# Optimization experiments

Measured on AMD Instinct MI355X. Metric: run time of the kernel, lower is better.

## Reference

```python
import jax, jax.numpy as jnp
import numpy as np

B, N, C, H = 4, 1024, 768, 12
D = C // H
SCALE = D ** -0.5


def setup_inputs() -> dict:
    key = jax.random.key(0)
    k1, k2, k3, k4 = jax.random.split(key, 4)
    x1 = jax.random.normal(k1, (B, N, C), dtype=jnp.float32)
    x2 = jax.random.normal(k2, (B, N, C), dtype=jnp.float32)
    # shared (dual-stream) Linear2 weights, torch nn.Linear layout: [out, in]
    W_qkv = jax.random.normal(k3, (3 * C, C), dtype=jnp.float32) * (C ** -0.5)
    b_qkv = jnp.zeros((3 * C,), dtype=jnp.float32)
    W_proj = jax.random.normal(k4, (C, C), dtype=jnp.float32) * (C ** -0.5)
    b_proj = jnp.zeros((C,), dtype=jnp.float32)
    return {"x1": x1, "x2": x2, "W_qkv": W_qkv, "b_qkv": b_qkv,
            "W_proj": W_proj, "b_proj": b_proj}


def _split_qkv(x, W_qkv, b_qkv):
    qkv = (x @ W_qkv.T + b_qkv).reshape(B, N, 3, H, D)
    qkv = jnp.transpose(qkv, (2, 0, 3, 1, 4))  # [3,B,H,N,D]
    return qkv[0], qkv[1], qkv[2]


def reference(x1, x2, W_qkv, b_qkv, W_proj, b_proj):
    q1, k1, v1 = _split_qkv(x1, W_qkv, b_qkv)
    q2, k2, v2 = _split_qkv(x2, W_qkv, b_qkv)
    # two score maps, combined before a single shared softmax
    s1 = jnp.einsum("bhqd,bhkd->bhqk", q1 * SCALE, k1)
    s2 = jnp.einsum("bhqd,bhkd->bhqk", q2 * SCALE, k2)
    attn = jax.nn.softmax(s1 + s2, axis=-1)  # [B,H,N,N]
    # same attention matrix applied to both value streams
    o1 = jnp.einsum("bhqk,bhkd->bhqd", attn, v1)
    o2 = jnpum = jnp.einsum("bhqk,bhkd->bhqd", attn, v2) if False else jnp.einsum("bhqk,bhkd->bhqd", attn, v2)
    o1 = jnp.transpose(o1, (0, 2, 1, 3)).reshape(B, N, C)
    o2 = jnp.transpose(o2, (0, 2, 1, 3)).reshape(B, N, C)
    y1 = o1 @ W_proj.T + b_proj
    y2 = o2 @ W_proj.T + b_proj
    return y1, y2
```

## Files before the change

### kernel.cpp

```cpp
#include <hip/hip_runtime.h>
#include <hip/hip_bf16.h>


typedef __bf16 bf16x8 __attribute__((ext_vector_type(8)));
typedef float  f32x4  __attribute__((ext_vector_type(4)));

__device__ __forceinline__ bf16x8 cvt8(const float* p) {
    f32x4 f0 = *(const f32x4*)p;
    f32x4 f1 = *(const f32x4*)(p + 4);
    bf16x8 r;
    r[0] = (__bf16)f0[0]; r[1] = (__bf16)f0[1]; r[2] = (__bf16)f0[2]; r[3] = (__bf16)f0[3];
    r[4] = (__bf16)f1[0]; r[5] = (__bf16)f1[1]; r[6] = (__bf16)f1[2]; r[7] = (__bf16)f1[3];
    return r;
}

__device__ __forceinline__ void async16(const __bf16* g, __bf16* l) {
    __builtin_amdgcn_global_load_lds(
        (const __attribute__((address_space(1))) void*)g,
        (__attribute__((address_space(3))) void*)l, 16, 0, 0);
}

__global__ __launch_bounds__(256)
void cvt_k(const float* __restrict__ src, __bf16* __restrict__ dst, int n) {
    int i = (blockIdx.x * 256 + threadIdx.x) * 8;
    if (i < n) *(bf16x8*)(dst + i) = cvt8(src + i);
}

__global__ __launch_bounds__(256)
void gemm_qkv_s(const __bf16* __restrict__ A, const __bf16* __restrict__ Wq,
                const float* __restrict__ bias,
                __bf16* __restrict__ qo, __bf16* __restrict__ ko,
                __bf16* __restrict__ vo, int st)
{
    constexpr int K = 768;
    __shared__ __bf16 As[128 * 32];
    __shared__ __bf16 Bs[128 * 32];

    const int t = threadIdx.x, w = t >> 6, lane = t & 63;
    const int l15 = lane & 15, quad = lane >> 4;
    const int wm = w >> 1, wn = w & 1;
    const int gx = blockIdx.x, gy = blockIdx.y;
    const int lrow = lane >> 2, lcol = (lane & 3) * 8;

    const __bf16* Ab = A  + (size_t)(gy * 128) * K;
    const __bf16* Bb = Wq + (size_t)(gx * 128) * K;

    f32x4 acc[4][4];
#pragma unroll
    for (int mi = 0; mi < 4; mi++)
#pragma unroll
        for (int ni = 0; ni < 4; ni++) acc[mi][ni] = f32x4{0.f, 0.f, 0.f, 0.f};

    for (int k0 = 0; k0 < K; k0 += 32) {
#pragma unroll
        for (int i = 0; i < 2; i++) {
            int r = w * 32 + i * 16 + lrow;
            async16(Ab + (size_t)r * K + k0 + lcol, &As[r * 32 + lcol]);
            async16(Bb + (size_t)r * K + k0 + lcol, &Bs[r * 32 + lcol]);
        }
        __syncthreads();
        bf16x8 af[4], bfr[4];
#pragma unroll
        for (int mi = 0; mi < 4; mi++)
            af[mi] = *(const bf16x8*)&As[(wm * 64 + mi * 16 + l15) * 32 + quad * 8];
#pragma unroll
        for (int ni = 0; ni < 4; ni++)
            bfr[ni] = *(const bf16x8*)&Bs[(wn * 64 + ni * 16 + l15) * 32 + quad * 8];
#pragma unroll
        for (int mi = 0; mi < 4; mi++)
#pragma unroll
            for (int ni = 0; ni < 4; ni++)
                acc[mi][ni] = __builtin_amdgcn_mfma_f32_16x16x32_bf16(af[mi], bfr[ni], acc[mi][ni], 0, 0, 0);
        __syncthreads();
    }

#pragma unroll
    for (int ni = 0; ni < 4; ni++) {
        int j     = gx * 128 + wn * 64 + ni * 16 + l15;
        int which = j / 768;
        int c     = j - which * 768;
        int h = c >> 6, d = c & 63;
        float bj  = bias[j];
#pragma unroll
        for (int mi = 0; mi < 4; mi++) {
#pragma unroll
            for (int r = 0; r < 4; r++) {
                int row = gy * 128 + wm * 64 + mi * 16 + quad * 4 + r;
                int b = row >> 10, tok = row & 1023;
                float val = acc[mi][ni][r] + bj;
                if (which == 0)
                    qo[((size_t)((st * 4 + b) * 12 + h) * 1024 + tok) * 64 + d] = (__bf16)(val * 0.125f);
                else if (which == 1)
                    ko[((size_t)((st * 4 + b) * 12 + h) * 1024 + tok) * 64 + d] = (__bf16)val;
                else
                    vo[((size_t)((st * 4 + b) * 12 + h) * 64 + d) * 1024 + tok] = (__bf16)val;
            }
        }
    }
}

__global__ __launch_bounds__(256)
void gemm_proj(const __bf16* __restrict__ A, const __bf16* __restrict__ Wp,
               const float* __restrict__ bias, float* __restrict__ out)
{
    constexpr int K = 768;
    __shared__ __bf16 As[128 * 32];
    __shared__ __bf16 Bs[128 * 32];

    const int t = threadIdx.x, w = t >> 6, lane = t & 63;
    const int l15 = lane & 15, quad = lane >> 4;
    const int wm = w >> 1, wn = w & 1;
    const int gx = blockIdx.x, gy = blockIdx.y;
    const int lrow = lane >> 2, lcol = (lane & 3) * 8;

    const __bf16* Ab = A  + (size_t)(gy * 128) * K;
    const __bf16* Bb = Wp + (size_t)(gx * 128) * K;

    f32x4 acc[4][4];
#pragma unroll
    for (int mi = 0; mi < 4; mi++)
#pragma unroll
        for (int ni = 0; ni < 4; ni++) acc[mi][ni] = f32x4{0.f, 0.f, 0.f, 0.f};

    for (int k0 = 0; k0 < K; k0 += 32) {
#pragma unroll
        for (int i = 0; i < 2; i++) {
            int r = w * 32 + i * 16 + lrow;
            async16(Ab + (size_t)r * K + k0 + lcol, &As[r * 32 + lcol]);
            async16(Bb + (size_t)r * K + k0 + lcol, &Bs[r * 32 + lcol]);
        }
        __syncthreads();
        bf16x8 af[4], bfr[4];
#pragma unroll
        for (int mi = 0; mi < 4; mi++)
            af[mi] = *(const bf16x8*)&As[(wm * 64 + mi * 16 + l15) * 32 + quad * 8];
#pragma unroll
        for (int ni = 0; ni < 4; ni++)
            bfr[ni] = *(const bf16x8*)&Bs[(wn * 64 + ni * 16 + l15) * 32 + quad * 8];
#pragma unroll
        for (int mi = 0; mi < 4; mi++)
#pragma unroll
            for (int ni = 0; ni < 4; ni++)
                acc[mi][ni] = __builtin_amdgcn_mfma_f32_16x16x32_bf16(af[mi], bfr[ni], acc[mi][ni], 0, 0, 0);
        __syncthreads();
    }

#pragma unroll
    for (int ni = 0; ni < 4; ni++) {
        int col  = gx * 128 + wn * 64 + ni * 16 + l15;
        float bj = bias[col];
#pragma unroll
        for (int mi = 0; mi < 4; mi++)
#pragma unroll
            for (int r = 0; r < 4; r++) {
                int row = gy * 128 + wm * 64 + mi * 16 + quad * 4 + r;
                out[(size_t)row * 768 + col] = acc[mi][ni][r] + bj;
            }
    }
}

__global__ __launch_bounds__(256)
void attn_k(const __bf16* __restrict__ qws, const __bf16* __restrict__ kws,
            const __bf16* __restrict__ vws, __bf16* __restrict__ ows)
{
    __shared__ __bf16 KVf[2][2][2][4][512];
    __shared__ __bf16 Ps[4][16 * 72];

    const int g  = blockIdx.x;
    const int qt = g / 48;
    const int bh = g % 48;
    const int b = bh / 12, h = bh % 12;
    const int t = threadIdx.x, w = t >> 6, lane = t & 63;
    const int l15 = lane & 15, quad = lane >> 4;

    const size_t head_off = (size_t)bh * 65536;
    const size_t ss       = (size_t)48 * 65536;

    bf16x8 qf[2][2];
#pragma unroll
    for (int s = 0; s < 2; s++)
#pragma unroll
        for (int kk = 0; kk < 2; kk++)
            qf[s][kk] = *(const bf16x8*)(qws + s * ss + head_off
                          + (size_t)(qt * 64 + w * 16 + l15) * 64 + kk * 32 + quad * 8);

    float m_prev = -1e30f, l_run = 0.f;
    f32x4 accO[2][4];
#pragma unroll
    for (int s = 0; s < 2; s++)
#pragma unroll
        for (int ni = 0; ni < 4; ni++) accO[s][ni] = f32x4{0.f, 0.f, 0.f, 0.f};

    const __bf16* kbase = kws + head_off;
    const __bf16* vbase = vws + head_off;

    for (int kt = 0; kt < 16; kt++) {
        __syncthreads();
#pragma unroll
        for (int i = 0; i < 8; i++) {
            int f  = w * 8 + i;
            int kv = f >> 4, s = (f >> 3) & 1, kk = (f >> 2) & 1, mi = f & 3;
            const __bf16* gp;
            if (kv == 0)
                gp = kbase + s * ss + (size_t)(kt * 64 + mi * 16 + l15) * 64
                     + kk * 32 + quad * 8;
            else
                gp = vbase + s * ss + (size_t)(mi * 16 + l15) * 1024
                     + kt * 64 + kk * 32 + quad * 8;
            async16(gp, &KVf[kv][s][kk][mi][lane * 8]);
        }
        __syncthreads();

        f32x4 accS[4];
#pragma unroll
        for (int i = 0; i < 4; i++) accS[i] = f32x4{0.f, 0.f, 0.f, 0.f};
#pragma unroll
        for (int s = 0; s < 2; s++)
#pragma unroll
            for (int kk = 0; kk < 2; kk++) {
                bf16x8 kf[4];
#pragma unroll
                for (int mi = 0; mi < 4; mi++)
                    kf[mi] = *(const bf16x8*)&KVf[0][s][kk][mi][lane * 8];
#pragma unroll
                for (int mi = 0; mi < 4; mi++)
                    accS[mi] = __builtin_amdgcn_mfma_f32_16x16x32_bf16(kf[mi], qf[s][kk], accS[mi], 0, 0, 0);
            }

        float mx = accS[0][0];
#pragma unroll
        for (int mi = 0; mi < 4; mi++)
#pragma unroll
            for (int r = 0; r < 4; r++) mx = fmaxf(mx, accS[mi][r]);
        mx = fmaxf(mx, __shfl_xor(mx, 16));
        mx = fmaxf(mx, __shfl_xor(mx, 32));
        float mnew  = fmaxf(m_prev, mx);
        float alpha = __expf(m_prev - mnew);
        float p[4][4], rs = 0.f;
#pragma unroll
        for (int mi = 0; mi < 4; mi++)
#pragma unroll
            for (int r = 0; r < 4; r++) {
                float pv = __expf(accS[mi][r] - mnew);
                p[mi][r] = pv;
                rs += pv;
            }
        rs += __shfl_xor(rs, 16);
        rs += __shfl_xor(rs, 32);
        l_run  = l_run * alpha + rs;
        m_prev = mnew;

        float alr[4];
#pragma unroll
        for (int r = 0; r < 4; r++) alr[r] = __shfl(alpha, quad * 4 + r);
#pragma unroll
        for (int s = 0; s < 2; s++)
#pragma unroll
            for (int ni = 0; ni < 4; ni++)
#pragma unroll
                for (int r = 0; r < 4; r++) accO[s][ni][r] *= alr[r];

#pragma unroll
        for (int mi = 0; mi < 4; mi++)
#pragma unroll
            for (int r = 0; r < 4; r++)
                Ps[w][l15 * 72 + mi * 16 + quad * 4 + r] = (__bf16)p[mi][r];

#pragma unroll
        for (int kk = 0; kk < 2; kk++) {
            bf16x8 pa = *(const bf16x8*)&Ps[w][l15 * 72 + kk * 32 + quad * 8];
#pragma unroll
            for (int s = 0; s < 2; s++)
#pragma unroll
                for (int ni = 0; ni < 4; ni++) {
                    bf16x8 vf = *(const bf16x8*)&KVf[1][s][kk][ni][lane * 8];
                    accO[s][ni] = __builtin_amdgcn_mfma_f32_16x16x32_bf16(pa, vf, accO[s][ni], 0, 0, 0);
                }
        }
    }

    float il = 1.f / l_run;
    float ilr[4];
#pragma unroll
    for (int r = 0; r < 4; r++) ilr[r] = __shfl(il, quad * 4 + r);
#pragma unroll
    for (int r = 0; r < 4; r++) {
        int tok = qt * 64 + w * 16 + quad * 4 + r;
#pragma unroll
        for (int s = 0; s < 2; s++)
#pragma unroll
            for (int ni = 0; ni < 4; ni++) {
                size_t idx = ((size_t)((s * 4 + b) * 1024 + tok)) * 768 + h * 64 + ni * 16 + l15;
                ows[idx] = (__bf16)(accO[s][ni][r] * ilr[r]);
            }
    }
}

extern "C" void kernel_launch(void* const* d_in, const int* in_sizes, int n_in,
                              void* d_out, int out_size, void* d_ws, size_t ws_size,
                              hipStream_t stream)
{
    const float* x1    = (const float*)d_in[0];
    const float* x2    = (const float*)d_in[1];
    const float* Wqkv  = (const float*)d_in[2];
    const float* bqkv  = (const float*)d_in[3];
    const float* Wproj = (const float*)d_in[4];
    const float* bproj = (const float*)d_in[5];
    float* out = (float*)d_out;

    const size_t qkv_elems = (size_t)2 * 4 * 12 * 1024 * 64;
    __bf16* q_ws = (__bf16*)d_ws;
    __bf16* k_ws = q_ws + qkv_elems;
    __bf16* v_ws = k_ws + qkv_elems;
    __bf16* pool = v_ws + qkv_elems;
    __bf16* Xc  = pool;
    __bf16* Wqc = pool + 3145728;
    __bf16* o_ws = pool;
    __bf16* Wpc = q_ws;

    cvt_k<<<1536, 256, 0, stream>>>(x1, Xc, 3145728);
    cvt_k<<<864,  256, 0, stream>>>(Wqkv, Wqc, 1769472);
    gemm_qkv_s<<<dim3(18, 32), 256, 0, stream>>>(Xc, Wqc, bqkv, q_ws, k_ws, v_ws, 0);
    cvt_k<<<1536, 256, 0, stream>>>(x2, Xc, 3145728);
    gemm_qkv_s<<<dim3(18, 32), 256, 0, stream>>>(Xc, Wqc, bqkv, q_ws, k_ws, v_ws, 1);
    attn_k<<<768, 256, 0, stream>>>(q_ws, k_ws, v_ws, o_ws);
    cvt_k<<<288, 256, 0, stream>>>(Wproj, Wpc, 589824);
    gemm_proj<<<dim3(6, 64), 256, 0, stream>>>(o_ws, Wpc, bproj, out);
}
```

Measured before the change: 250.1 us.

## Deepen GEMM K-tile to 64 and load V directly to registers in attention

Both GEMM kernels now stage a 64-wide K slice per iteration instead of 32, halving the number of barrier pairs and loop iterations while doubling LDS use. In the attention kernel, each wave loads V fragments straight from global memory into registers instead of going through shared memory, so only K is staged in LDS. P is written to LDS as packed 4-element bf16 vectors. The V change raises register pressure, and each wave now reads the full V tile redundantly from global or cache.

```diff
diff --git a/kernel.cpp b/kernel.cpp
--- a/kernel.cpp
+++ b/kernel.cpp
@@ -3,6 +3,7 @@
 
 
 typedef __bf16 bf16x8 __attribute__((ext_vector_type(8)));
+typedef __bf16 bf16x4 __attribute__((ext_vector_type(4)));
 typedef float  f32x4  __attribute__((ext_vector_type(4)));
 
 __device__ __forceinline__ bf16x8 cvt8(const float* p) {
@@ -33,14 +34,15 @@
                 __bf16* __restrict__ vo, int st)
 {
     constexpr int K = 768;
-    __shared__ __bf16 As[128 * 32];
-    __shared__ __bf16 Bs[128 * 32];
+    __shared__ __bf16 As[128 * 64];
+    __shared__ __bf16 Bs[128 * 64];
 
     const int t = threadIdx.x, w = t >> 6, lane = t & 63;
     const int l15 = lane & 15, quad = lane >> 4;
     const int wm = w >> 1, wn = w & 1;
     const int gx = blockIdx.x, gy = blockIdx.y;
-    const int lrow = lane >> 2, lcol = (lane & 3) * 8;
+    const int srow = w * 32 + (lane >> 3);
+    const int scol = (lane & 7) * 8;
 
     const __bf16* Ab = A  + (size_t)(gy * 128) * K;
     const __bf16* Bb = Wq + (size_t)(gx * 128) * K;
@@ -51,26 +53,29 @@
 #pragma unroll
         for (int ni = 0; ni < 4; ni++) acc[mi][ni] = f32x4{0.f, 0.f, 0.f, 0.f};
 
-    for (int k0 = 0; k0 < K; k0 += 32) {
-#pragma unroll
-        for (int i = 0; i < 2; i++) {
-            int r = w * 32 + i * 16 + lrow;
-            async16(Ab + (size_t)r * K + k0 + lcol, &As[r * 32 + lcol]);
-            async16(Bb + (size_t)r * K + k0 + lcol, &Bs[r * 32 + lcol]);
-        }
-        __syncthreads();
-        bf16x8 af[4], bfr[4];
-#pragma unroll
-        for (int mi = 0; mi < 4; mi++)
-            af[mi] = *(const bf16x8*)&As[(wm * 64 + mi * 16 + l15) * 32 + quad * 8];
-#pragma unroll
-        for (int ni = 0; ni < 4; ni++)
-            bfr[ni] = *(const bf16x8*)&Bs[(wn * 64 + ni * 16 + l15) * 32 + quad * 8];
-#pragma unroll
-        for (int mi = 0; mi < 4; mi++)
+    for (int k0 = 0; k0 < K; k0 += 64) {
+#pragma unroll
+        for (int i = 0; i < 4; i++) {
+            int r = srow + i * 8;
+            async16(Ab + (size_t)r * K + k0 + scol, &As[r * 64 + scol]);
+            async16(Bb + (size_t)r * K + k0 + scol, &Bs[r * 64 + scol]);
+        }
+        __syncthreads();
+#pragma unroll
+        for (int kk = 0; kk < 2; kk++) {
+            bf16x8 af[4], bfr[4];
+#pragma unroll
+            for (int mi = 0; mi < 4; mi++)
+                af[mi] = *(const bf16x8*)&As[(wm * 64 + mi * 16 + l15) * 64 + kk * 32 + quad * 8];
 #pragma unroll
             for (int ni = 0; ni < 4; ni++)
-                acc[mi][ni] = __builtin_amdgcn_mfma_f32_16x16x32_bf16(af[mi], bfr[ni], acc[mi][ni], 0, 0, 0);
+                bfr[ni] = *(const bf16x8*)&Bs[(wn * 64 + ni * 16 + l15) * 64 + kk * 32 + quad * 8];
+#pragma unroll
+            for (int mi = 0; mi < 4; mi++)
+#pragma unroll
+                for (int ni = 0; ni < 4; ni++)
+                    acc[mi][ni] = __builtin_amdgcn_mfma_f32_16x16x32_bf16(af[mi], bfr[ni], acc[mi][ni], 0, 0, 0);
+        }
         __syncthreads();
     }
 
@@ -104,14 +109,15 @@
                const float* __restrict__ bias, float* __restrict__ out)
 {
     constexpr int K = 768;
-    __shared__ __bf16 As[128 * 32];
-    __shared__ __bf16 Bs[128 * 32];
+    __shared__ __bf16 As[128 * 64];
+    __shared__ __bf16 Bs[128 * 64];
 
     const int t = threadIdx.x, w = t >> 6, lane = t & 63;
     const int l15 = lane & 15, quad = lane >> 4;
     const int wm = w >> 1, wn = w & 1;
     const int gx = blockIdx.x, gy = blockIdx.y;
-    const int lrow = lane >> 2, lcol = (lane & 3) * 8;
+    const int srow = w * 32 + (lane >> 3);
+    const int scol = (lane & 7) * 8;
 
     const __bf16* Ab = A  + (size_t)(gy * 128) * K;
     const __bf16* Bb = Wp + (size_t)(gx * 128) * K;
@@ -122,26 +128,29 @@
 #pragma unroll
         for (int ni = 0; ni < 4; ni++) acc[mi][ni] = f32x4{0.f, 0.f, 0.f, 0.f};
 
-    for (int k0 = 0; k0 < K; k0 += 32) {
-#pragma unroll
-        for (int i = 0; i < 2; i++) {
-            int r = w * 32 + i * 16 + lrow;
-            async16(Ab + (size_t)r * K + k0 + lcol, &As[r * 32 + lcol]);
-            async16(Bb + (size_t)r * K + k0 + lcol, &Bs[r * 32 + lcol]);
-        }
-        __syncthreads();
-        bf16x8 af[4], bfr[4];
-#pragma unroll
-        for (int mi = 0; mi < 4; mi++)
-            af[mi] = *(const bf16x8*)&As[(wm * 64 + mi * 16 + l15) * 32 + quad * 8];
-#pragma unroll
-        for (int ni = 0; ni < 4; ni++)
-            bfr[ni] = *(const bf16x8*)&Bs[(wn * 64 + ni * 16 + l15) * 32 + quad * 8];
-#pragma unroll
-        for (int mi = 0; mi < 4; mi++)
+    for (int k0 = 0; k0 < K; k0 += 64) {
+#pragma unroll
+        for (int i = 0; i < 4; i++) {
+            int r = srow + i * 8;
+            async16(Ab + (size_t)r * K + k0 + scol, &As[r * 64 + scol]);
+            async16(Bb + (size_t)r * K + k0 + scol, &Bs[r * 64 + scol]);
+        }
+        __syncthreads();
+#pragma unroll
+        for (int kk = 0; kk < 2; kk++) {
+            bf16x8 af[4], bfr[4];
+#pragma unroll
+            for (int mi = 0; mi < 4; mi++)
+                af[mi] = *(const bf16x8*)&As[(wm * 64 + mi * 16 + l15) * 64 + kk * 32 + quad * 8];
 #pragma unroll
             for (int ni = 0; ni < 4; ni++)
-                acc[mi][ni] = __builtin_amdgcn_mfma_f32_16x16x32_bf16(af[mi], bfr[ni], acc[mi][ni], 0, 0, 0);
+                bfr[ni] = *(const bf16x8*)&Bs[(wn * 64 + ni * 16 + l15) * 64 + kk * 32 + quad * 8];
+#pragma unroll
+            for (int mi = 0; mi < 4; mi++)
+#pragma unroll
+                for (int ni = 0; ni < 4; ni++)
+                    acc[mi][ni] = __builtin_amdgcn_mfma_f32_16x16x32_bf16(af[mi], bfr[ni], acc[mi][ni], 0, 0, 0);
+        }
         __syncthreads();
     }
 
@@ -163,7 +172,7 @@
 void attn_k(const __bf16* __restrict__ qws, const __bf16* __restrict__ kws,
             const __bf16* __restrict__ vws, __bf16* __restrict__ ows)
 {
-    __shared__ __bf16 KVf[2][2][2][4][512];
+    __shared__ __bf16 Kf[2][2][4][512];
     __shared__ __bf16 Ps[4][16 * 72];
 
     const int g  = blockIdx.x;
@@ -197,18 +206,23 @@
     for (int kt = 0; kt < 16; kt++) {
         __syncthreads();
 #pragma unroll
-        for (int i = 0; i < 8; i++) {
-            int f  = w * 8 + i;
-            int kv = f >> 4, s = (f >> 3) & 1, kk = (f >> 2) & 1, mi = f & 3;
-            const __bf16* gp;
-            if (kv == 0)
-                gp = kbase + s * ss + (size_t)(kt * 64 + mi * 16 + l15) * 64
-                     + kk * 32 + quad * 8;
-            else
-                gp = vbase + s * ss + (size_t)(mi * 16 + l15) * 1024
-                     + kt * 64 + kk * 32 + quad * 8;
-            async16(gp, &KVf[kv][s][kk][mi][lane * 8]);
-        }
+        for (int i = 0; i < 4; i++) {
+            int f = w * 4 + i;
+            int s = f >> 3, kk = (f >> 2) & 1, mi = f & 3;
+            async16(kbase + s * ss + (size_t)(kt * 64 + mi * 16 + l15) * 64
+                        + kk * 32 + quad * 8,
+                    &Kf[s][kk][mi][lane * 8]);
+        }
+        bf16x8 vf[2][2][4];
+#pragma unroll
+        for (int s = 0; s < 2; s++)
+#pragma unroll
+            for (int kk = 0; kk < 2; kk++)
+#pragma unroll
+                for (int ni = 0; ni < 4; ni++)
+                    vf[s][kk][ni] = *(const bf16x8*)(vbase + s * ss
+                                      + (size_t)(ni * 16 + l15) * 1024
+                                      + kt * 64 + kk * 32 + quad * 8);
         __syncthreads();
 
         f32x4 accS[4];
@@ -221,7 +235,7 @@
                 bf16x8 kf[4];
 #pragma unroll
                 for (int mi = 0; mi < 4; mi++)
-                    kf[mi] = *(const bf16x8*)&KVf[0][s][kk][mi][lane * 8];
+                    kf[mi] = *(const bf16x8*)&Kf[s][kk][mi][lane * 8];
 #pragma unroll
                 for (int mi = 0; mi < 4; mi++)
                     accS[mi] = __builtin_amdgcn_mfma_f32_16x16x32_bf16(kf[mi], qf[s][kk], accS[mi], 0, 0, 0);
@@ -236,15 +250,17 @@
         mx = fmaxf(mx, __shfl_xor(mx, 32));
         float mnew  = fmaxf(m_prev, mx);
         float alpha = __expf(m_prev - mnew);
-        float p[4][4], rs = 0.f;
-#pragma unroll
-        for (int mi = 0; mi < 4; mi++)
+        float rs = 0.f;
+        bf16x4 pk[4];
+#pragma unroll
+        for (int mi = 0; mi < 4; mi++) {
 #pragma unroll
             for (int r = 0; r < 4; r++) {
                 float pv = __expf(accS[mi][r] - mnew);
-                p[mi][r] = pv;
+                pk[mi][r] = (__bf16)pv;
                 rs += pv;
             }
+        }
         rs += __shfl_xor(rs, 16);
         rs += __shfl_xor(rs, 32);
         l_run  = l_run * alpha + rs;
@@ -262,9 +278,7 @@
 
 #pragma unroll
         for (int mi = 0; mi < 4; mi++)
-#pragma unroll
-            for (int r = 0; r < 4; r++)
-                Ps[w][l15 * 72 + mi * 16 + quad * 4 + r] = (__bf16)p[mi][r];
+            *(bf16x4*)&Ps[w][l15 * 72 + mi * 16 + quad * 4] = pk[mi];
 
 #pragma unroll
         for (int kk = 0; kk < 2; kk++) {
@@ -272,10 +286,8 @@
 #pragma unroll
             for (int s = 0; s < 2; s++)
 #pragma unroll
-                for (int ni = 0; ni < 4; ni++) {
-                    bf16x8 vf = *(const bf16x8*)&KVf[1][s][kk][ni][lane * 8];
-                    accO[s][ni] = __builtin_amdgcn_mfma_f32_16x16x32_bf16(pa, vf, accO[s][ni], 0, 0, 0);
-                }
+                for (int ni = 0; ni < 4; ni++)
+                    accO[s][ni] = __builtin_amdgcn_mfma_f32_16x16x32_bf16(pa, vf[s][kk][ni], accO[s][ni], 0, 0, 0);
         }
     }
 
```

After: 343.2 us. 1.37x slower.
